# Performance work log

Measured on AMD Instinct MI355X. Metric: run time of the kernel, lower is better.

## Reference

```python
import jax, jax.numpy as jnp
import numpy as np

N, D, NUM_CLASSES = 4096, 1024, 1000


def setup_inputs() -> dict:
    key = jax.random.key(0)
    k1, k2 = jax.random.split(key)
    output = jax.random.normal(k1, (N, D), dtype=jnp.float32)
    target = jax.random.randint(k2, (N,), 0, NUM_CLASSES, dtype=jnp.int64)
    return {"output": output, "target": target}


def reference(output, target):
    # k1: strictly-lower-triangular part of the gram matrix [N, N]
    gram = output @ output.T
    k1 = jnp.tril(gram, -1)
    # k2: strictly-lower-triangular label-equality mask (vectorized form of
    # the original O(N^2) python double loop)
    eq = (target[:, None] == target[None, :]).astype(output.dtype)
    k2 = jnp.tril(eq, -1)
    return -(jnp.sum(k1 * k2) / (jnp.sum(k2) * jnp.linalg.norm(k1)))
```

## Files before the change

kernel.cpp:

```cpp
#include <hip/hip_runtime.h>
#include <hip/hip_bf16.h>


typedef __attribute__((ext_vector_type(8))) short short8;
typedef __attribute__((ext_vector_type(4))) float f32x4;

#define N_ROWS 4096
#define D_DIM  1024
#define N_CLS  1000
#define NTILE  32
#define NBLK   528
#define NK     32

__device__ __forceinline__ unsigned short f2bf(float f) {
  unsigned u = __float_as_uint(f);
  u += 0x7fffu + ((u >> 16) & 1u);
  return (unsigned short)(u >> 16);
}

__device__ __forceinline__ void gload16(const short* g, const char* l) {
  __builtin_amdgcn_global_load_lds(
      (const __attribute__((address_space(1))) unsigned*)g,
      (__attribute__((address_space(3))) unsigned*)(void*)l, 16, 0, 0);
}

__global__ void __launch_bounds__(256) kconvrow(const float* __restrict__ A,
                                                short* __restrict__ Ab,
                                                double* __restrict__ rowp) {
  __shared__ double wr2[4];
  const int tid = threadIdx.x, lane = tid & 63, w = tid >> 6;
  const int row0 = blockIdx.x * 8;
  double ls = 0.0;
#pragma unroll
  for (int rr = 0; rr < 2; ++rr) {
    const int i = row0 + w * 2 + rr;
    const float4* src = (const float4*)(A + (size_t)i * D_DIM);
    short4* dst = (short4*)(Ab + (size_t)i * D_DIM);
    float s = 0.f;
#pragma unroll
    for (int c = 0; c < 4; ++c) {
      const float4 v = src[lane + c * 64];
      s += v.x * v.x + v.y * v.y + v.z * v.z + v.w * v.w;
      short4 o;
      o.x = (short)f2bf(v.x); o.y = (short)f2bf(v.y);
      o.z = (short)f2bf(v.z); o.w = (short)f2bf(v.w);
      dst[lane + c * 64] = o;
    }
#pragma unroll
    for (int off = 32; off; off >>= 1) s += __shfl_down(s, off);
    if (lane == 0) ls += (double)s;
  }
  if (lane == 0) wr2[w] = ls;
  __syncthreads();
  if (tid == 0) rowp[blockIdx.x] = wr2[0] + wr2[1] + wr2[2] + wr2[3];
}

__global__ void __launch_bounds__(256) kclass(const float* __restrict__ A,
                                              const int* __restrict__ target,
                                              double* __restrict__ cssp,
                                              int* __restrict__ cntp) {
  __shared__ int list[N_ROWS];
  __shared__ int lcnt;
  __shared__ float wred[4];
  const int c = blockIdx.x, tid = threadIdx.x;
  if (tid == 0) lcnt = 0;
  __syncthreads();
  for (int j = tid; j < N_ROWS; j += 256)
    if (target[j] == c) { int p = atomicAdd(&lcnt, 1); list[p] = j; }
  __syncthreads();
  const int n = lcnt;
  float4 acc = make_float4(0.f, 0.f, 0.f, 0.f);
  for (int m = 0; m < n; ++m) {
    const float4 v = *(const float4*)(A + (size_t)list[m] * D_DIM + tid * 4);
    acc.x += v.x; acc.y += v.y; acc.z += v.z; acc.w += v.w;
  }
  float s = acc.x * acc.x + acc.y * acc.y + acc.z * acc.z + acc.w * acc.w;
#pragma unroll
  for (int off = 32; off; off >>= 1) s += __shfl_down(s, off);
  const int lane = tid & 63, wid = tid >> 6;
  if (lane == 0) wred[wid] = s;
  __syncthreads();
  if (tid == 0) {
    cssp[c] = (double)(wred[0] + wred[1] + wred[2] + wred[3]);
    cntp[c] = n;
  }
}

__global__ void __launch_bounds__(512, 4) kfrob(const short* __restrict__ Ab,
                                                double* __restrict__ frobp) {
  __shared__ __align__(16) short As[128 * 32];
  __shared__ __align__(16) short Bs[128 * 32];
  __shared__ double wred[8];
  const int tid = threadIdx.x, lane = tid & 63, w = tid >> 6;

  const int b = blockIdx.x;
  int bi = (int)((sqrtf(8.f * (float)b + 1.f) - 1.f) * 0.5f);
  while ((bi + 1) * (bi + 2) / 2 <= b) ++bi;
  while (bi * (bi + 1) / 2 > b) --bi;
  const int bj = b - bi * (bi + 1) / 2;
  const bool diag = (bi == bj);

  const short* Pa = Ab + (size_t)(bi * 128) * D_DIM;
  const short* Pb = Ab + (size_t)(bj * 128) * D_DIM;

  f32x4 acc[4][2];
#pragma unroll
  for (int m = 0; m < 4; ++m)
#pragma unroll
    for (int n = 0; n < 2; ++n) acc[m][n] = (f32x4){0.f, 0.f, 0.f, 0.f};

  const int wr = w >> 2, wc = w & 3;
  const int row16 = lane & 15, ko = (lane >> 4) * 8;

  const int sr = tid >> 2, sc = tid & 3;
  const size_t gofs = (size_t)sr * D_DIM + sc * 8;
  const int lofs = w * 1024;

  for (int k0 = 0; k0 < D_DIM; k0 += 32) {
    gload16(Pa + gofs + k0, (const char*)As + lofs);
    gload16(Pb + gofs + k0, (const char*)Bs + lofs);
    __syncthreads();
    short8 af[4], bf[2];
#pragma unroll
    for (int m = 0; m < 4; ++m)
      af[m] = *(const short8*)&As[(wr * 64 + m * 16 + row16) * 32 + ko];
#pragma unroll
    for (int n = 0; n < 2; ++n)
      bf[n] = *(const short8*)&Bs[(wc * 32 + n * 16 + row16) * 32 + ko];
#pragma unroll
    for (int m = 0; m < 4; ++m)
#pragma unroll
      for (int n = 0; n < 2; ++n)
        acc[m][n] = __builtin_amdgcn_mfma_f32_16x16x32_bf16(af[m], bf[n], acc[m][n], 0, 0, 0);
    __syncthreads();
  }

  float fs = 0.f;
  if (!diag) {
#pragma unroll
    for (int m = 0; m < 4; ++m)
#pragma unroll
      for (int n = 0; n < 2; ++n)
#pragma unroll
        for (int q = 0; q < 4; ++q) fs += acc[m][n][q] * acc[m][n][q];
  } else {
    const int rbase = (lane >> 4) * 4, cbase = lane & 15;
#pragma unroll
    for (int m = 0; m < 4; ++m)
#pragma unroll
      for (int n = 0; n < 2; ++n)
#pragma unroll
        for (int q = 0; q < 4; ++q) {
          const int rl = wr * 64 + m * 16 + rbase + q;
          const int cl = wc * 32 + n * 16 + cbase;
          if (rl > cl) fs += acc[m][n][q] * acc[m][n][q];
        }
  }
#pragma unroll
  for (int off = 32; off; off >>= 1) fs += __shfl_down(fs, off);
  if (lane == 0) wred[w] = (double)fs;
  __syncthreads();
  if (tid == 0) {
    double t = 0.0;
#pragma unroll
    for (int i = 0; i < 8; ++i) t += wred[i];
    frobp[b] = t;
  }
}

__global__ void __launch_bounds__(256) kfinal(const double* __restrict__ rowp,
                                              const double* __restrict__ cssp,
                                              const int* __restrict__ cntp,
                                              const double* __restrict__ frobp,
                                              float* __restrict__ out) {
  __shared__ double red[256];
  const int tid = threadIdx.x;
  double lsum = rowp[tid] + rowp[tid + 256];
  double lcss = 0.0, lcnn = 0.0, lfr = 0.0;
  for (int c = tid; c < N_CLS; c += 256) {
    lcss += cssp[c];
    const double nc = (double)cntp[c];
    lcnn += nc * nc;
  }
  for (int c = tid; c < NBLK; c += 256) lfr += frobp[c];

  double vals[4] = {lsum, lcss, lcnn, lfr};
  double res[4];
  for (int v = 0; v < 4; ++v) {
    red[tid] = vals[v];
    __syncthreads();
    for (int s = 128; s; s >>= 1) {
      if (tid < s) red[tid] += red[tid + s];
      __syncthreads();
    }
    res[v] = red[0];
    __syncthreads();
  }
  if (tid == 0) {
    const double sumr = res[0], css = res[1], cnn = res[2], frob = res[3];
    const double S1 = 0.5 * (css - sumr);
    const double S2 = 0.5 * (cnn - (double)N_ROWS);
    const double S3 = frob;
    out[0] = (float)(-(S1 / (S2 * sqrt(S3))));
  }
}

extern "C" void kernel_launch(void* const* d_in, const int* in_sizes, int n_in,
                              void* d_out, int out_size, void* d_ws, size_t ws_size,
                              hipStream_t stream) {
  const float* A = (const float*)d_in[0];
  const int* target = (const int*)d_in[1];
  float* out = (float*)d_out;

  char* ws = (char*)d_ws;
  short*  Ab    = (short*)ws;
  double* rowp  = (double*)(ws + 8388608);
  double* cssp  = (double*)(ws + 8388608 + 4096);
  int*    cntp  = (int*)   (ws + 8388608 + 4096 + 8000);
  double* frobp = (double*)(ws + 8388608 + 4096 + 8000 + 4096);

  kconvrow<<<512, 256, 0, stream>>>(A, Ab, rowp);
  kclass<<<N_CLS, 256, 0, stream>>>(A, target, cssp, cntp);
  kfrob<<<NBLK, 512, 0, stream>>>(Ab, frobp);
  kfinal<<<1, 256, 0, stream>>>(rowp, cssp, cntp, frobp, out);
}
```

Before: 52.82 us.

## Fuse kernels into two launches and pipeline the gram GEMM with swizzled LDS

Merges the bf16 conversion and per-class kernels into one launch. The separate final reduction becomes a last-block-done step at the end of the gram kernel, guarded by an atomic counter. The gram kernel moves to 256 threads with 4x4 accumulator tiles per wave, K=64 double-buffered LDS stages and an XOR swizzle against bank conflicts. It also adds MFMA priority hints and a block-index remap for L2 locality. These are meant to cut launch overhead and global-load latency stalls, at the cost of more register and LDS pressure and the correctness risk of cross-block atomics.

Result: slower. 61.54 us (+16.5%).

```diff
diff --git a/kernel.cpp b/kernel.cpp
--- a/kernel.cpp
+++ b/kernel.cpp
@@ -8,9 +8,8 @@
 #define N_ROWS 4096
 #define D_DIM  1024
 #define N_CLS  1000
-#define NTILE  32
 #define NBLK   528
-#define NK     32
+#define NKT    16
 
 __device__ __forceinline__ unsigned short f2bf(float f) {
   unsigned u = __float_as_uint(f);
@@ -24,76 +23,83 @@
       (__attribute__((address_space(3))) unsigned*)(void*)l, 16, 0, 0);
 }
 
-__global__ void __launch_bounds__(256) kconvrow(const float* __restrict__ A,
-                                                short* __restrict__ Ab,
-                                                double* __restrict__ rowp) {
-  __shared__ double wr2[4];
+__global__ void __launch_bounds__(256) kconv(const float* __restrict__ A,
+                                             const int* __restrict__ target,
+                                             short* __restrict__ Ab,
+                                             double* __restrict__ rowp,
+                                             double* __restrict__ cssp,
+                                             int* __restrict__ cntp,
+                                             unsigned* __restrict__ done) {
   const int tid = threadIdx.x, lane = tid & 63, w = tid >> 6;
-  const int row0 = blockIdx.x * 8;
-  double ls = 0.0;
-#pragma unroll
-  for (int rr = 0; rr < 2; ++rr) {
-    const int i = row0 + w * 2 + rr;
-    const float4* src = (const float4*)(A + (size_t)i * D_DIM);
-    short4* dst = (short4*)(Ab + (size_t)i * D_DIM);
-    float s = 0.f;
-#pragma unroll
-    for (int c = 0; c < 4; ++c) {
-      const float4 v = src[lane + c * 64];
-      s += v.x * v.x + v.y * v.y + v.z * v.z + v.w * v.w;
-      short4 o;
-      o.x = (short)f2bf(v.x); o.y = (short)f2bf(v.y);
-      o.z = (short)f2bf(v.z); o.w = (short)f2bf(v.w);
-      dst[lane + c * 64] = o;
-    }
+
+  if (blockIdx.x < 512) {
+    if (blockIdx.x == 0 && tid == 0) *done = 0u;
+    __shared__ double wr2[4];
+    const int row0 = blockIdx.x * 8;
+    double ls = 0.0;
+#pragma unroll
+    for (int rr = 0; rr < 2; ++rr) {
+      const int i = row0 + w * 2 + rr;
+      const float4* src = (const float4*)(A + (size_t)i * D_DIM);
+      short4* dst = (short4*)(Ab + (size_t)i * D_DIM);
+      float s = 0.f;
+#pragma unroll
+      for (int c = 0; c < 4; ++c) {
+        const float4 v = src[lane + c * 64];
+        s += v.x * v.x + v.y * v.y + v.z * v.z + v.w * v.w;
+        short4 o;
+        o.x = (short)f2bf(v.x); o.y = (short)f2bf(v.y);
+        o.z = (short)f2bf(v.z); o.w = (short)f2bf(v.w);
+        dst[lane + c * 64] = o;
+      }
+#pragma unroll
+      for (int off = 32; off; off >>= 1) s += __shfl_down(s, off);
+      if (lane == 0) ls += (double)s;
+    }
+    if (lane == 0) wr2[w] = ls;
+    __syncthreads();
+    if (tid == 0) rowp[blockIdx.x] = wr2[0] + wr2[1] + wr2[2] + wr2[3];
+  } else {
+    __shared__ int list[N_ROWS];
+    __shared__ int lcnt;
+    __shared__ float wred[4];
+    const int c = blockIdx.x - 512;
+    if (c >= N_CLS) return;
+    if (tid == 0) lcnt = 0;
+    __syncthreads();
+    for (int j = tid; j < N_ROWS; j += 256)
+      if (target[j] == c) { int p = atomicAdd(&lcnt, 1); list[p] = j; }
+    __syncthreads();
+    const int n = lcnt;
+    float4 acc = make_float4(0.f, 0.f, 0.f, 0.f);
+    for (int m = 0; m < n; ++m) {
+      const float4 v = *(const float4*)(A + (size_t)list[m] * D_DIM + tid * 4);
+      acc.x += v.x; acc.y += v.y; acc.z += v.z; acc.w += v.w;
+    }
+    float s = acc.x * acc.x + acc.y * acc.y + acc.z * acc.z + acc.w * acc.w;
 #pragma unroll
     for (int off = 32; off; off >>= 1) s += __shfl_down(s, off);
-    if (lane == 0) ls += (double)s;
-  }
-  if (lane == 0) wr2[w] = ls;
-  __syncthreads();
-  if (tid == 0) rowp[blockIdx.x] = wr2[0] + wr2[1] + wr2[2] + wr2[3];
-}
-
-__global__ void __launch_bounds__(256) kclass(const float* __restrict__ A,
-                                              const int* __restrict__ target,
-                                              double* __restrict__ cssp,
-                                              int* __restrict__ cntp) {
-  __shared__ int list[N_ROWS];
-  __shared__ int lcnt;
-  __shared__ float wred[4];
-  const int c = blockIdx.x, tid = threadIdx.x;
-  if (tid == 0) lcnt = 0;
-  __syncthreads();
-  for (int j = tid; j < N_ROWS; j += 256)
-    if (target[j] == c) { int p = atomicAdd(&lcnt, 1); list[p] = j; }
-  __syncthreads();
-  const int n = lcnt;
-  float4 acc = make_float4(0.f, 0.f, 0.f, 0.f);
-  for (int m = 0; m < n; ++m) {
-    const float4 v = *(const float4*)(A + (size_t)list[m] * D_DIM + tid * 4);
-    acc.x += v.x; acc.y += v.y; acc.z += v.z; acc.w += v.w;
-  }
-  float s = acc.x * acc.x + acc.y * acc.y + acc.z * acc.z + acc.w * acc.w;
-#pragma unroll
-  for (int off = 32; off; off >>= 1) s += __shfl_down(s, off);
-  const int lane = tid & 63, wid = tid >> 6;
-  if (lane == 0) wred[wid] = s;
-  __syncthreads();
-  if (tid == 0) {
-    cssp[c] = (double)(wred[0] + wred[1] + wred[2] + wred[3]);
-    cntp[c] = n;
-  }
-}
-
-__global__ void __launch_bounds__(512, 4) kfrob(const short* __restrict__ Ab,
-                                                double* __restrict__ frobp) {
-  __shared__ __align__(16) short As[128 * 32];
-  __shared__ __align__(16) short Bs[128 * 32];
-  __shared__ double wred[8];
+    if (lane == 0) wred[w] = s;
+    __syncthreads();
+    if (tid == 0) {
+      cssp[c] = (double)(wred[0] + wred[1] + wred[2] + wred[3]);
+      cntp[c] = n;
+    }
+  }
+}
+
+__global__ void __launch_bounds__(256, 2) kgram(const short* __restrict__ Ab,
+                                                double* __restrict__ frobp,
+                                                const double* __restrict__ rowp,
+                                                const double* __restrict__ cssp,
+                                                const int* __restrict__ cntp,
+                                                unsigned* __restrict__ done,
+                                                float* __restrict__ out) {
+  __shared__ __align__(16) short As[2][128 * 64];
+  __shared__ __align__(16) short Bs[2][128 * 64];
   const int tid = threadIdx.x, lane = tid & 63, w = tid >> 6;
 
-  const int b = blockIdx.x;
+  const int b = (blockIdx.x & 7) * 66 + (blockIdx.x >> 3);
   int bi = (int)((sqrtf(8.f * (float)b + 1.f) - 1.f) * 0.5f);
   while ((bi + 1) * (bi + 2) / 2 <= b) ++bi;
   while (bi * (bi + 1) / 2 > b) --bi;
@@ -103,44 +109,95 @@
   const short* Pa = Ab + (size_t)(bi * 128) * D_DIM;
   const short* Pb = Ab + (size_t)(bj * 128) * D_DIM;
 
-  f32x4 acc[4][2];
+  f32x4 acc[4][4];
 #pragma unroll
   for (int m = 0; m < 4; ++m)
 #pragma unroll
-    for (int n = 0; n < 2; ++n) acc[m][n] = (f32x4){0.f, 0.f, 0.f, 0.f};
-
-  const int wr = w >> 2, wc = w & 3;
-  const int row16 = lane & 15, ko = (lane >> 4) * 8;
-
-  const int sr = tid >> 2, sc = tid & 3;
-  const size_t gofs = (size_t)sr * D_DIM + sc * 8;
-  const int lofs = w * 1024;
-
-  for (int k0 = 0; k0 < D_DIM; k0 += 32) {
-    gload16(Pa + gofs + k0, (const char*)As + lofs);
-    gload16(Pb + gofs + k0, (const char*)Bs + lofs);
-    __syncthreads();
-    short8 af[4], bf[2];
-#pragma unroll
-    for (int m = 0; m < 4; ++m)
-      af[m] = *(const short8*)&As[(wr * 64 + m * 16 + row16) * 32 + ko];
-#pragma unroll
-    for (int n = 0; n < 2; ++n)
-      bf[n] = *(const short8*)&Bs[(wc * 32 + n * 16 + row16) * 32 + ko];
-#pragma unroll
-    for (int m = 0; m < 4; ++m)
+    for (int n = 0; n < 4; ++n) acc[m][n] = (f32x4){0.f, 0.f, 0.f, 0.f};
+
+  const int wm = w >> 1, wn = w & 1;
+  const int row16 = lane & 15, ck = lane >> 4;
+
+  const int srow = tid >> 3;
+  const int scol = (tid & 7) ^ (srow & 7);
+
+#define STAGE4(P, BASE, kt)                                                 \
+  do {                                                                      \
+    _Pragma("unroll")                                                       \
+    for (int i = 0; i < 4; ++i)                                             \
+      gload16((P) + (size_t)(i * 32 + srow) * D_DIM + (kt) * 64 + scol * 8, \
+              (BASE) + i * 4096 + w * 1024);                                \
+  } while (0)
+
+#define FRAG(BASE, R, ks)                                                   \
+  (*(const short8*)((const char*)(BASE) + (R) * 128 +                       \
+                    ((((ks) * 4 + ck) ^ ((R) & 7)) << 4)))
+
+  STAGE4(Pa, (char*)As[0], 0);
+  STAGE4(Pb, (char*)Bs[0], 0);
+  asm volatile("s_waitcnt vmcnt(0)" ::: "memory");
+  __builtin_amdgcn_sched_barrier(0);
+  __builtin_amdgcn_s_barrier();
+
+  int cur = 0;
+#pragma unroll 1
+  for (int t = 0; t < NKT; ++t) {
+    short8 a[2][4], bb[2][4];
+#pragma unroll
+    for (int ks = 0; ks < 2; ++ks)
+#pragma unroll
+      for (int m = 0; m < 4; ++m)
+        a[ks][m] = FRAG(As[cur], wm * 64 + m * 16 + row16, ks);
+#pragma unroll
+    for (int ks = 0; ks < 2; ++ks)
 #pragma unroll
       for (int n = 0; n < 2; ++n)
-        acc[m][n] = __builtin_amdgcn_mfma_f32_16x16x32_bf16(af[m], bf[n], acc[m][n], 0, 0, 0);
-    __syncthreads();
-  }
+        bb[ks][n] = FRAG(Bs[cur], wn * 64 + n * 16 + row16, ks);
+    if (t < NKT - 1) STAGE4(Pa, (char*)As[cur ^ 1], t + 1);
+    __builtin_amdgcn_s_barrier();
+    __builtin_amdgcn_s_setprio(1);
+#pragma unroll
+    for (int ks = 0; ks < 2; ++ks)
+#pragma unroll
+      for (int m = 0; m < 4; ++m)
+#pragma unroll
+        for (int n = 0; n < 2; ++n)
+          acc[m][n] = __builtin_amdgcn_mfma_f32_16x16x32_bf16(
+              a[ks][m], bb[ks][n], acc[m][n], 0, 0, 0);
+    __builtin_amdgcn_s_setprio(0);
+    __builtin_amdgcn_s_barrier();
+#pragma unroll
+    for (int ks = 0; ks < 2; ++ks)
+#pragma unroll
+      for (int n = 0; n < 2; ++n)
+        bb[ks][n] = FRAG(Bs[cur], wn * 64 + (n + 2) * 16 + row16, ks);
+    if (t < NKT - 1) STAGE4(Pb, (char*)Bs[cur ^ 1], t + 1);
+    __builtin_amdgcn_s_barrier();
+    __builtin_amdgcn_s_setprio(1);
+#pragma unroll
+    for (int ks = 0; ks < 2; ++ks)
+#pragma unroll
+      for (int m = 0; m < 4; ++m)
+#pragma unroll
+        for (int n = 0; n < 2; ++n)
+          acc[m][n + 2] = __builtin_amdgcn_mfma_f32_16x16x32_bf16(
+              a[ks][m], bb[ks][n], acc[m][n + 2], 0, 0, 0);
+    __builtin_amdgcn_s_setprio(0);
+    __builtin_amdgcn_s_barrier();
+    asm volatile("s_waitcnt vmcnt(0)" ::: "memory");
+    __builtin_amdgcn_sched_barrier(0);
+    __builtin_amdgcn_s_barrier();
+    cur ^= 1;
+  }
+#undef STAGE4
+#undef FRAG
 
   float fs = 0.f;
   if (!diag) {
 #pragma unroll
     for (int m = 0; m < 4; ++m)
 #pragma unroll
-      for (int n = 0; n < 2; ++n)
+      for (int n = 0; n < 4; ++n)
 #pragma unroll
         for (int q = 0; q < 4; ++q) fs += acc[m][n][q] * acc[m][n][q];
   } else {
@@ -148,33 +205,30 @@
 #pragma unroll
     for (int m = 0; m < 4; ++m)
 #pragma unroll
-      for (int n = 0; n < 2; ++n)
+      for (int n = 0; n < 4; ++n)
 #pragma unroll
         for (int q = 0; q < 4; ++q) {
-          const int rl = wr * 64 + m * 16 + rbase + q;
-          const int cl = wc * 32 + n * 16 + cbase;
+          const int rl = wm * 64 + m * 16 + rbase + q;
+          const int cl = wn * 64 + n * 16 + cbase;
           if (rl > cl) fs += acc[m][n][q] * acc[m][n][q];
         }
   }
 #pragma unroll
   for (int off = 32; off; off >>= 1) fs += __shfl_down(fs, off);
-  if (lane == 0) wred[w] = (double)fs;
+
+  __syncthreads();
+  double* red = (double*)As;
+  __shared__ bool last;
+  if (lane == 0) red[w] = (double)fs;
   __syncthreads();
   if (tid == 0) {
-    double t = 0.0;
-#pragma unroll
-    for (int i = 0; i < 8; ++i) t += wred[i];
-    frobp[b] = t;
-  }
-}
-
-__global__ void __launch_bounds__(256) kfinal(const double* __restrict__ rowp,
-                                              const double* __restrict__ cssp,
-                                              const int* __restrict__ cntp,
-                                              const double* __restrict__ frobp,
-                                              float* __restrict__ out) {
-  __shared__ double red[256];
-  const int tid = threadIdx.x;
+    frobp[b] = red[0] + red[1] + red[2] + red[3];
+    __threadfence();
+    last = (atomicAdd(done, 1u) == NBLK - 1);
+  }
+  __syncthreads();
+  if (!last) return;
+
   double lsum = rowp[tid] + rowp[tid + 256];
   double lcss = 0.0, lcnn = 0.0, lfr = 0.0;
   for (int c = tid; c < N_CLS; c += 256) {
@@ -182,8 +236,8 @@
     const double nc = (double)cntp[c];
     lcnn += nc * nc;
   }
-  for (int c = tid; c < NBLK; c += 256) lfr += frobp[c];
-
+  for (int c = tid; c < NBLK; c += 256)
+    lfr += atomicAdd(&frobp[c], 0.0);
   double vals[4] = {lsum, lcss, lcnn, lfr};
   double res[4];
   for (int v = 0; v < 4; ++v) {
@@ -197,11 +251,9 @@
     __syncthreads();
   }
   if (tid == 0) {
-    const double sumr = res[0], css = res[1], cnn = res[2], frob = res[3];
-    const double S1 = 0.5 * (css - sumr);
-    const double S2 = 0.5 * (cnn - (double)N_ROWS);
-    const double S3 = frob;
-    out[0] = (float)(-(S1 / (S2 * sqrt(S3))));
+    const double S1 = 0.5 * (res[1] - res[0]);
+    const double S2 = 0.5 * (res[2] - (double)N_ROWS);
+    out[0] = (float)(-(S1 / (S2 * sqrt(res[3]))));
   }
 }
 
@@ -213,14 +265,13 @@
   float* out = (float*)d_out;
 
   char* ws = (char*)d_ws;
-  short*  Ab    = (short*)ws;
-  double* rowp  = (double*)(ws + 8388608);
-  double* cssp  = (double*)(ws + 8388608 + 4096);
-  int*    cntp  = (int*)   (ws + 8388608 + 4096 + 8000);
-  double* frobp = (double*)(ws + 8388608 + 4096 + 8000 + 4096);
-
-  kconvrow<<<512, 256, 0, stream>>>(A, Ab, rowp);
-  kclass<<<N_CLS, 256, 0, stream>>>(A, target, cssp, cntp);
-  kfrob<<<NBLK, 512, 0, stream>>>(Ab, frobp);
-  kfinal<<<1, 256, 0, stream>>>(rowp, cssp, cntp, frobp, out);
-}
+  short*    Ab    = (short*)ws;
+  double*   rowp  = (double*)(ws + 8388608);
+  double*   cssp  = (double*)(ws + 8392704);
+  int*      cntp  = (int*)   (ws + 8400704);
+  double*   frobp = (double*)(ws + 8404736);
+  unsigned* done  = (unsigned*)(ws + 8408960);
+
+  kconv<<<512 + N_CLS, 256, 0, stream>>>(A, target, Ab, rowp, cssp, cntp, done);
+  kgram<<<NBLK, 256, 0, stream>>>(Ab, frobp, rowp, cssp, cntp, done, out);
+}
```
